# Performance work log

Hardware: AMD Instinct MI355X
Metric: run time of the kernel (lower is better)

The kernel has to match this reference:

```python
import jax, jax.numpy as jnp
import numpy as np

B, S, H, L, NH, DH, FF = 64, 256, 768, 12, 12, 64, 3072
V, MAXP, NTYPE, NI, NS = 30522, 512, 2, 10, 64


def setup_inputs() -> dict:
    key = jax.random.key(0)
    ks = iter(jax.random.split(key, 40))
    n = lambda shp, s=0.02: jax.random.normal(next(ks), shp, jnp.float32) * s
    inp = {
        'input_ids': jax.random.randint(next(ks), (B, S), 0, V),
        'attention_mask': jnp.ones((B, S), jnp.int32),
        'token_type_ids': jnp.zeros((B, S), jnp.int32),
        'intent_labels': jax.random.randint(next(ks), (B,), 0, NI),
        'slot_labels': jax.random.randint(next(ks), (B, S), 0, NS),
        'word_emb': n((V, H)), 'pos_emb': n((MAXP, H)), 'type_emb': n((NTYPE, H)),
        'emb_ln_g': jnp.ones((H,)), 'emb_ln_b': jnp.zeros((H,)),
        'Wq': n((L, H, H)), 'bq': jnp.zeros((L, H)),
        'Wk': n((L, H, H)), 'bk': jnp.zeros((L, H)),
        'Wv': n((L, H, H)), 'bv': jnp.zeros((L, H)),
        'Wo': n((L, H, H)), 'bo': jnp.zeros((L, H)),
        'ln1_g': jnp.ones((L, H)), 'ln1_b': jnp.zeros((L, H)),
        'W1': n((L, H, FF)), 'b1': jnp.zeros((L, FF)),
        'W2': n((L, FF, H)), 'b2': jnp.zeros((L, H)),
        'ln2_g': jnp.ones((L, H)), 'ln2_b': jnp.zeros((L, H)),
        'Wi': n((H, NI)), 'bi': jnp.zeros((NI,)),
        'Ws': n((H, NS)), 'bs': jnp.zeros((NS,)),
        'crf_start': n((NS,), 0.1), 'crf_end': n((NS,), 0.1),
        'crf_trans': n((NS, NS), 0.1),
    }
    return inp


def _ln(x, g, b):
    m = x.mean(-1, keepdims=True)
    v = jnp.square(x - m).mean(-1, keepdims=True)
    return (x - m) * jax.lax.rsqrt(v + 1e-12) * g + b


def _forward(params, input_ids, attention_mask, token_type_ids, intent_labels, slot_labels):
    (word_emb, pos_emb, type_emb, emb_ln_g, emb_ln_b,
     Wq, bq, Wk, bk, Wv, bv, Wo, bo, ln1_g, ln1_b,
     W1, b1, W2, b2, ln2_g, ln2_b,
     Wi, bi, Ws, bs, crf_start, crf_end, crf_trans) = params
    Bn, Sn = input_ids.shape
    Hn = word_emb.shape[1]
    dh = Hn // NH
    # BERT embeddings (dropout is identity in eval)
    x = word_emb[input_ids] + pos_emb[:Sn][None] + type_emb[token_type_ids]
    x = _ln(x, emb_ln_g, emb_ln_b)
    bias = (1.0 - attention_mask.astype(x.dtype))[:, None, None, :] * -1e9  # [B,1,1,S]

    def layer(h, p):
        wq, cq, wk, ck, wv, cv, wo, co, g1, d1, w1, e1, w2, e2, g2, d2 = p
        q = (h @ wq + cq).reshape(Bn, Sn, NH, dh)
        k = (h @ wk + ck).reshape(Bn, Sn, NH, dh)
        v = (h @ wv + cv).reshape(Bn, Sn, NH, dh)
        sc = jnp.einsum('bqnd,bknd->bnqk', q, k) / jnp.sqrt(jnp.float32(dh)) + bias
        a = jax.nn.softmax(sc, axis=-1)
        ctx = jnp.einsum('bnqk,bknd->bqnd', a, v).reshape(Bn, Sn, Hn)
        h2 = _ln(h + ctx @ wo + co, g1, d1)
        ff = jax.nn.gelu(h2 @ w1 + e1, approximate=False)
        return _ln(h2 + ff @ w2 + e2, g2, d2), None

    x, _ = jax.lax.scan(layer, x, (Wq, bq, Wk, bk, Wv, bv, Wo, bo,
                                   ln1_g, ln1_b, W1, b1, W2, b2, ln2_g, ln2_b))
    intent_logits = x[:, 0, :] @ Wi + bi           # [B, NI]
    slot_logits = x @ Ws + bs                      # [B, S, NS]
    # intent cross-entropy (mean over batch)
    lp = jax.nn.log_softmax(intent_logits, axis=-1)
    intent_loss = -jnp.take_along_axis(lp, intent_labels[:, None], axis=1).mean()
    # CRF log-likelihood
    mask = attention_mask.astype(slot_logits.dtype)
    em, tags = slot_logits, slot_labels
    t0 = tags[:, 0]
    score = crf_start[t0] + jnp.take_along_axis(em[:, 0, :], t0[:, None], axis=1)[:, 0]
    prev, cur = tags[:, :-1], tags[:, 1:]
    step_sc = crf_trans[prev, cur] + jnp.take_along_axis(em[:, 1:, :], cur[..., None], axis=2)[..., 0]
    score = score + (step_sc * mask[:, 1:]).sum(1)
    lengths = attention_mask.sum(1)
    last_tag = jnp.take_along_axis(tags, (lengths - 1)[:, None].astype(tags.dtype), axis=1)[:, 0]
    score = score + crf_end[last_tag]
    em_t = jnp.swapaxes(em, 0, 1)    # [S,B,C]
    mk_t = jnp.swapaxes(mask, 0, 1)  # [S,B]
    alpha0 = crf_start[None, :] + em_t[0]

    def crf_step(alpha, xs):
        e, m = xs
        nxt = jax.scipy.special.logsumexp(alpha[:, :, None] + crf_trans[None], axis=1) + e
        return jnp.where(m[:, None] > 0, nxt, alpha), None

    alpha, _ = jax.lax.scan(crf_step, alpha0, (em_t[1:], mk_t[1:]))
    logZ = jax.scipy.special.logsumexp(alpha + crf_end[None, :], axis=1)
    llh = score - logZ                # per-sequence log-likelihood
    crf_loss = -llh.mean()
    return intent_loss + 2.0 * crf_loss


def reference(input_ids, attention_mask, token_type_ids, intent_labels, slot_labels,
              word_emb, pos_emb, type_emb, emb_ln_g, emb_ln_b,
              Wq, bq, Wk, bk, Wv, bv, Wo, bo, ln1_g, ln1_b,
              W1, b1, W2, b2, ln2_g, ln2_b,
              Wi, bi, Ws, bs, crf_start, crf_end, crf_trans):
    params = (word_emb, pos_emb, type_emb, emb_ln_g, emb_ln_b,
              Wq, bq, Wk, bk, Wv, bv, Wo, bo, ln1_g, ln1_b,
              W1, b1, W2, b2, ln2_g, ln2_b,
              Wi, bi, Ws, bs, crf_start, crf_end, crf_trans)
    return _forward(params, input_ids, attention_mask, token_type_ids, intent_labels, slot_labels)
```

## Files before the change

### kernel.cpp

```cpp
#include <hip/hip_runtime.h>
#include <stdint.h>

typedef unsigned short u16;
typedef __attribute__((ext_vector_type(8))) short bh8;
typedef __attribute__((ext_vector_type(4))) float f4;

#define DEV static __device__ __forceinline__

DEV u16 f2bf(float f){ union{float f; uint32_t u;} v; v.f=f; uint32_t r=v.u + 0x7FFFu + ((v.u>>16)&1u); return (u16)(r>>16); }
DEV float bf2f(u16 u){ union{uint32_t u; float f;} v; v.u=((uint32_t)u)<<16; return v.f; }

DEV void mfma16(f4& d, bh8 a, bh8 b){
  asm("v_mfma_f32_16x16x32_bf16 %0, %1, %2, %0" : "+v"(d) : "v"(a), "v"(b));
}

#define FENCE16(A) asm volatile("s_nop 7\ns_nop 7" : \
 "+v"(A[0][0]),"+v"(A[0][1]),"+v"(A[0][2]),"+v"(A[0][3]),\
 "+v"(A[1][0]),"+v"(A[1][1]),"+v"(A[1][2]),"+v"(A[1][3]),\
 "+v"(A[2][0]),"+v"(A[2][1]),"+v"(A[2][2]),"+v"(A[2][3]),\
 "+v"(A[3][0]),"+v"(A[3][1]),"+v"(A[3][2]),"+v"(A[3][3]))

#define GLD16(g,l) __builtin_amdgcn_global_load_lds( \
    (__attribute__((address_space(1))) void*)(void*)(g), \
    (__attribute__((address_space(3))) void*)(void*)(l), 16, 0, 0)

struct GemmP { const u16* A; const u16* B; int K; void* C; int ldc;
               const float* b0; const float* b1; const float* b2; const u16* res; };

template<int EPI>
__global__ __launch_bounds__(256)
void gemm_bt(GemmP p){
  __shared__ __align__(16) u16 As[128*32];
  __shared__ __align__(16) u16 Bs[128*32];
  const int t=threadIdx.x, l=t&63, w=t>>6, wr=w>>1, wc=w&1;
  const int m0=blockIdx.x*128, n0=blockIdx.y*128;
  const u16* Ab = p.A + (size_t)m0*p.K;
  const u16* Bb = p.B + (size_t)n0*p.K;
  const int srow=l>>2, scol=(l&3)*8;
  f4 acc[4][4] = {};
  for(int k0=0;k0<p.K;k0+=32){
#pragma unroll
    for(int i=0;i<2;i++){
      const int c=w*2+i;
      GLD16(Ab + (size_t)(c*16+srow)*p.K + k0 + scol, &As[c*512]);
      GLD16(Bb + (size_t)(c*16+srow)*p.K + k0 + scol, &Bs[c*512]);
    }
    __syncthreads();
    bh8 af[4], bfr[4];
#pragma unroll
    for(int m=0;m<4;m++) af[m] = *(const bh8*)&As[(wr*64+m*16+(l&15))*32 + (l>>4)*8];
#pragma unroll
    for(int n=0;n<4;n++) bfr[n] = *(const bh8*)&Bs[(wc*64+n*16+(l&15))*32 + (l>>4)*8];
#pragma unroll
    for(int m=0;m<4;m++)
#pragma unroll
      for(int n=0;n<4;n++) mfma16(acc[m][n], af[m], bfr[n]);
    __syncthreads();
  }
  FENCE16(acc);
  const int lc=l&15, lr=(l>>4)*4;
#pragma unroll
  for(int m=0;m<4;m++)
#pragma unroll
  for(int n=0;n<4;n++)
#pragma unroll
  for(int r=0;r<4;r++){
    const int gr = m0 + wr*64 + m*16 + lr + r;
    const int gc = n0 + wc*64 + n*16 + lc;
    float v = acc[m][n][r];
    if(EPI==0){
      const float* bp = (gc<768)? p.b0 : (gc<1536? p.b1 : p.b2);
      const int bc = (gc<768)? gc : (gc<1536? gc-768 : gc-1536);
      ((u16*)p.C)[(size_t)gr*p.ldc + gc] = f2bf(v + bp[bc]);
    } else if(EPI==1){
      v += p.b0[gc] + bf2f(p.res[(size_t)gr*p.ldc + gc]);
      ((u16*)p.C)[(size_t)gr*p.ldc + gc] = f2bf(v);
    } else if(EPI==2){
      v += p.b0[gc];
      v = 0.5f*v*(1.f + erff(v*0.70710678118f));
      ((u16*)p.C)[(size_t)gr*p.ldc + gc] = f2bf(v);
    } else {
      v += (gc<64)? p.b0[gc] : 0.f;
      ((float*)p.C)[(size_t)gr*p.ldc + gc] = v;
    }
  }
}

__global__ __launch_bounds__(256)
void attn_kernel(const u16* __restrict__ qkv, const int* __restrict__ amask, u16* __restrict__ ctx){
  __shared__ __align__(16) u16 Ks[256*64];
  __shared__ __align__(16) u16 Vt[64*256];
  __shared__ __align__(16) u16 Ps[4*64*64];
  __shared__ float biasS[256];
  const int t=threadIdx.x, l=t&63, w=t>>6;
  const int b=blockIdx.x/12, h=blockIdx.x%12;
  biasS[t] = (1.f - (float)amask[b*256+t]) * -1e9f;
  const u16* kb = qkv + ((size_t)b*256)*2304 + 768 + h*64;
  const u16* vb = kb + 768;
#pragma unroll
  for(int i=0;i<8;i++){
    const int c = t + i*256;
    const int row = c>>3, seg = c&7;
    uint4 kv = *(const uint4*)(kb + (size_t)row*2304 + seg*8);
    const int ba = row*128 + seg*16;
    *(uint4*)((char*)Ks + (ba ^ ((row&7)<<4))) = kv;
    uint4 vv = *(const uint4*)(vb + (size_t)row*2304 + seg*8);
    const u16* pv = (const u16*)&vv;
#pragma unroll
    for(int j=0;j<8;j++){
      const int d = seg*8+j;
      const int bb = d*512 + row*2;
      *(u16*)((char*)Vt + (bb ^ ((d&7)<<4))) = pv[j];
    }
  }
  bh8 aq[4][2];
  const u16* qb = qkv + ((size_t)b*256 + w*64)*2304 + h*64;
#pragma unroll
  for(int m=0;m<4;m++)
#pragma unroll
    for(int ks=0;ks<2;ks++)
      aq[m][ks] = *(const bh8*)(qb + (size_t)(m*16+(l&15))*2304 + ks*32 + (l>>4)*8);
  __syncthreads();
  float mrun[4][4], lrun[4][4];
  f4 o[4][4] = {};
#pragma unroll
  for(int m=0;m<4;m++)
#pragma unroll
    for(int r=0;r<4;r++){ mrun[m][r] = -3e38f; lrun[m][r]=0.f; }
  u16* Pw = Ps + w*4096;
  for(int kt=0;kt<4;kt++){
    f4 sacc[4][4] = {};
#pragma unroll
    for(int ks=0;ks<2;ks++)
#pragma unroll
      for(int n=0;n<4;n++){
        const int row = kt*64 + n*16 + (l&15);
        const int by = row*128 + ks*64 + (l>>4)*16;
        bh8 bk = *(const bh8*)((const char*)Ks + (by ^ ((row&7)<<4)));
#pragma unroll
        for(int m=0;m<4;m++) mfma16(sacc[m][n], aq[m][ks], bk);
      }
    FENCE16(sacc);
#pragma unroll
    for(int m=0;m<4;m++){
      float rmax[4] = {-3e38f,-3e38f,-3e38f,-3e38f};
#pragma unroll
      for(int n=0;n<4;n++){
        const float bi = biasS[kt*64 + n*16 + (l&15)];
#pragma unroll
        for(int r=0;r<4;r++){
          float sv = sacc[m][n][r]*0.125f + bi;
          sacc[m][n][r] = sv;
          rmax[r] = fmaxf(rmax[r], sv);
        }
      }
#pragma unroll
      for(int dd=1; dd<16; dd<<=1)
#pragma unroll
        for(int r=0;r<4;r++) rmax[r] = fmaxf(rmax[r], __shfl_xor(rmax[r], dd));
      float psum[4];
#pragma unroll
      for(int r=0;r<4;r++){
        const float mn = fmaxf(mrun[m][r], rmax[r]);
        const float corr = __expf(mrun[m][r] - mn);
        mrun[m][r] = mn;
        lrun[m][r] *= corr;
#pragma unroll
        for(int nd=0; nd<4; nd++) o[m][nd][r] *= corr;
        psum[r] = 0.f;
      }
#pragma unroll
      for(int n=0;n<4;n++)
#pragma unroll
        for(int r=0;r<4;r++){
          const float pvv = __expf(sacc[m][n][r] - mrun[m][r]);
          sacc[m][n][r] = pvv;
          psum[r] += pvv;
        }
#pragma unroll
      for(int dd=1; dd<16; dd<<=1)
#pragma unroll
        for(int r=0;r<4;r++) psum[r] += __shfl_xor(psum[r], dd);
#pragma unroll
      for(int r=0;r<4;r++) lrun[m][r] += psum[r];
#pragma unroll
      for(int n=0;n<4;n++)
#pragma unroll
        for(int r=0;r<4;r++){
          const int prow = m*16 + (l>>4)*4 + r;
          const int pcol = n*16 + (l&15);
          const int by = prow*128 + pcol*2;
          *(u16*)((char*)Pw + (by ^ ((prow&7)<<4))) = f2bf(sacc[m][n][r]);
        }
    }
#pragma unroll
    for(int ks=0;ks<2;ks++){
      bh8 ap[4];
#pragma unroll
      for(int m=0;m<4;m++){
        const int prow = m*16 + (l&15);
        const int by = prow*128 + (ks*32 + (l>>4)*8)*2;
        ap[m] = *(const bh8*)((const char*)Pw + (by ^ ((prow&7)<<4)));
      }
#pragma unroll
      for(int nd=0; nd<4; nd++){
        const int dR = nd*16 + (l&15);
        const int by = dR*512 + (kt*64 + ks*32 + (l>>4)*8)*2;
        bh8 bv = *(const bh8*)((const char*)Vt + (by ^ ((dR&7)<<4)));
#pragma unroll
        for(int m=0;m<4;m++) mfma16(o[m][nd], ap[m], bv);
      }
    }
  }
  FENCE16(o);
#pragma unroll
  for(int m=0;m<4;m++)
#pragma unroll
  for(int nd=0; nd<4; nd++)
#pragma unroll
  for(int r=0;r<4;r++){
    const int row = w*64 + m*16 + (l>>4)*4 + r;
    const float vv = o[m][nd][r] / lrun[m][r];
    ctx[((size_t)b*256 + row)*768 + h*64 + nd*16 + (l&15)] = f2bf(vv);
  }
}

__global__ void ln_kernel(const u16* __restrict__ in, const float* __restrict__ g,
                          const float* __restrict__ b, u16* __restrict__ out){
  const int row = blockIdx.x, t = threadIdx.x;
  __shared__ float red[8];
  const u16* rp = in + (size_t)row*768;
  float v[3]; float s=0.f, q=0.f;
#pragma unroll
  for(int i=0;i<3;i++){ float x = bf2f(rp[t + i*256]); v[i]=x; s+=x; q+=x*x; }
#pragma unroll
  for(int dd=1; dd<64; dd<<=1){ s += __shfl_xor(s,dd); q += __shfl_xor(q,dd); }
  if((t&63)==0){ red[t>>6]=s; red[4+(t>>6)]=q; }
  __syncthreads();
  s = red[0]+red[1]+red[2]+red[3];
  q = red[4]+red[5]+red[6]+red[7];
  const float mean = s*(1.f/768.f);
  float var = q*(1.f/768.f) - mean*mean; var = fmaxf(var, 0.f);
  const float rs = rsqrtf(var + 1e-12f);
  u16* op = out + (size_t)row*768;
#pragma unroll
  for(int i=0;i<3;i++){ const int hh=t+i*256; op[hh] = f2bf((v[i]-mean)*rs*g[hh] + b[hh]); }
}

__global__ void embed_ln(const int* __restrict__ ids, const int* __restrict__ tti,
    const float* __restrict__ we, const float* __restrict__ pe, const float* __restrict__ te,
    const float* __restrict__ g, const float* __restrict__ bb, u16* __restrict__ x){
  const int tok = blockIdx.x, t = threadIdx.x;
  __shared__ float red[8];
  const int id = ids[tok], tyid = tti[tok], s0 = tok & 255;
  float v[3]; float s=0.f,q=0.f;
#pragma unroll
  for(int i=0;i<3;i++){
    const int hh = t+i*256;
    float x0 = we[(size_t)id*768+hh] + pe[(size_t)s0*768+hh] + te[(size_t)tyid*768+hh];
    v[i]=x0; s+=x0; q+=x0*x0;
  }
#pragma unroll
  for(int dd=1; dd<64; dd<<=1){ s += __shfl_xor(s,dd); q += __shfl_xor(q,dd); }
  if((t&63)==0){ red[t>>6]=s; red[4+(t>>6)]=q; }
  __syncthreads();
  s = red[0]+red[1]+red[2]+red[3];
  q = red[4]+red[5]+red[6]+red[7];
  const float mean = s*(1.f/768.f);
  float var = q*(1.f/768.f) - mean*mean; var = fmaxf(var, 0.f);
  const float rs = rsqrtf(var + 1e-12f);
#pragma unroll
  for(int i=0;i<3;i++){ const int hh=t+i*256; x[(size_t)tok*768+hh] = f2bf((v[i]-mean)*rs*g[hh] + bb[hh]); }
}

__global__ void transpose_cvt(const float* __restrict__ src, u16* __restrict__ dst, int R, int C){
  __shared__ float sm[32][33];
  const int ntc = C>>5;
  const int tr = blockIdx.x/ntc, tc = blockIdx.x - tr*ntc;
  const int r0 = tr<<5, c0 = tc<<5;
  const int tx = threadIdx.x, ty2 = threadIdx.y;
#pragma unroll
  for(int i=0;i<4;i++) sm[ty2+i*8][tx] = src[(size_t)(r0+ty2+i*8)*C + c0+tx];
  __syncthreads();
#pragma unroll
  for(int i=0;i<4;i++) dst[(size_t)(c0+ty2+i*8)*R + r0+tx] = f2bf(sm[tx][ty2+i*8]);
}

__global__ void conv_layer(const float* __restrict__ Wq, const float* __restrict__ Wk,
    const float* __restrict__ Wv, const float* __restrict__ Wo,
    const float* __restrict__ W1, const float* __restrict__ W2, u16* __restrict__ Wt){
  __shared__ float sm[32][33];
  const int bid = blockIdx.x;
  const float* src; u16* dst; int R, C, tt;
  if(bid<2304){
    R=768; C=768; const int mi = bid/576; tt = bid - mi*576;
    src = (mi==0?Wq: mi==1?Wk: mi==2?Wv: Wo);
    dst = Wt + (size_t)mi*589824;
  } else if(bid<4608){ R=768; C=3072; tt=bid-2304; src=W1; dst=Wt+2359296; }
  else { R=3072; C=768; tt=bid-4608; src=W2; dst=Wt+4718592; }
  const int ntc=C>>5; const int tr=tt/ntc, tc=tt-tr*ntc;
  const int r0=tr<<5, c0=tc<<5, tx=threadIdx.x, ty2=threadIdx.y;
#pragma unroll
  for(int i=0;i<4;i++) sm[ty2+i*8][tx] = src[(size_t)(r0+ty2+i*8)*C + c0+tx];
  __syncthreads();
#pragma unroll
  for(int i=0;i<4;i++) dst[(size_t)(c0+ty2+i*8)*R + r0+tx] = f2bf(sm[tx][ty2+i*8]);
}

__global__ void intent_kernel(const u16* __restrict__ x, const float* __restrict__ Wi,
    const float* __restrict__ bi, const int* __restrict__ lab, float* __restrict__ parts){
  const int b = blockIdx.x, t = threadIdx.x;
  __shared__ float xs[768];
  __shared__ float lg[10];
  const u16* rp = x + ((size_t)b*256)*768;
#pragma unroll
  for(int i=0;i<3;i++) xs[t+i*256] = bf2f(rp[t+i*256]);
  __syncthreads();
  if(t<10){
    float s = bi[t];
    for(int k=0;k<768;k++) s += xs[k]*Wi[(size_t)k*10 + t];
    lg[t] = s;
  }
  __syncthreads();
  if(t==0){
    float m = lg[0];
    for(int j=1;j<10;j++) m = fmaxf(m, lg[j]);
    float se = 0.f;
    for(int j=0;j<10;j++) se += expf(lg[j]-m);
    parts[b] = (logf(se) + m) - lg[lab[b]];
  }
}

__global__ __launch_bounds__(64)
void crf_kernel(const float* __restrict__ em, const int* __restrict__ tags,
    const int* __restrict__ amask, const float* __restrict__ cs, const float* __restrict__ ce,
    const float* __restrict__ tr, float* __restrict__ parts){
  const int b = blockIdx.x, j = threadIdx.x;
  const float* eb = em + (size_t)b*256*128;
  const int* tg = tags + b*256;
  const int* mk = amask + b*256;
  __shared__ __align__(16) float aS[64];
  float Etr[64];
#pragma unroll
  for(int i=0;i<64;i++) Etr[i] = __expf(tr[i*64 + j]);
  float sc = 0.f; int len = 0;
  for(int s=j+1; s<256; s+=64){
    const int pv = tg[s-1], cu = tg[s];
    sc += (tr[pv*64+cu] + eb[(size_t)s*128+cu]) * (float)mk[s];
  }
  for(int s=j; s<256; s+=64) len += mk[s];
#pragma unroll
  for(int dd=1; dd<64; dd<<=1){ sc += __shfl_xor(sc,dd); len += __shfl_xor(len,dd); }
  const int t0 = tg[0];
  float score = sc + cs[t0] + eb[t0] + ce[tg[len-1]];
  float a = __expf(cs[j] + eb[j]);
  float logc = 0.f;
  float em_s = eb[128 + j];
  int   mk_s = mk[1];
  for(int s=1; s<256; s++){
    const int sn = (s<255)? s+1 : s;
    const float em_n = eb[(size_t)sn*128 + j];
    const int   mk_n = mk[sn];
    aS[j] = a;
    __syncthreads();
    float acc0=0.f, acc1=0.f, acc2=0.f, acc3=0.f;
    const float4* ap = (const float4*)aS;
#pragma unroll
    for(int q2=0;q2<16;q2++){
      const float4 av = ap[q2];
      acc0 += av.x*Etr[4*q2+0];
      acc1 += av.y*Etr[4*q2+1];
      acc2 += av.z*Etr[4*q2+2];
      acc3 += av.w*Etr[4*q2+3];
    }
    __syncthreads();
    const float nxt = ((acc0+acc1)+(acc2+acc3)) * __expf(em_s);
    a = (mk_s > 0) ? nxt : a;
    if((s&7)==7){
      const float c = __shfl(a, 0);
      logc += __logf(c);
      a *= (1.f/c);
    }
    em_s = em_n; mk_s = mk_n;
  }
  float v2 = logf(a) + logc + ce[j];
  float am2 = v2;
#pragma unroll
  for(int dd=1; dd<64; dd<<=1) am2 = fmaxf(am2, __shfl_xor(am2,dd));
  float se = __expf(v2 - am2);
#pragma unroll
  for(int dd=1; dd<64; dd<<=1) se += __shfl_xor(se,dd);
  if(j==0) parts[64+b] = (logf(se)+am2) - score;
}

__global__ void final_reduce(const float* __restrict__ parts, float* __restrict__ out){
  const int t = threadIdx.x;
  float a = parts[t], c = parts[64+t];
#pragma unroll
  for(int dd=1; dd<64; dd<<=1){ a += __shfl_xor(a,dd); c += __shfl_xor(c,dd); }
  if(t==0) out[0] = a*(1.f/64.f) + 2.f*c*(1.f/64.f);
}

extern "C" void kernel_launch(void* const* d_in, const int* in_sizes, int n_in,
                              void* d_out, int out_size, void* d_ws, size_t ws_size,
                              hipStream_t stream){
  (void)in_sizes; (void)n_in; (void)out_size;
  const int* ids   = (const int*)d_in[0];
  const int* amask = (const int*)d_in[1];
  const int* tti   = (const int*)d_in[2];
  const int* ilab  = (const int*)d_in[3];
  const int* slab  = (const int*)d_in[4];
  const float* we  = (const float*)d_in[5];
  const float* pe  = (const float*)d_in[6];
  const float* te  = (const float*)d_in[7];
  const float* eg  = (const float*)d_in[8];
  const float* ebt = (const float*)d_in[9];
  const float* Wq  = (const float*)d_in[10];
  const float* bq  = (const float*)d_in[11];
  const float* Wk  = (const float*)d_in[12];
  const float* bkk = (const float*)d_in[13];
  const float* Wv  = (const float*)d_in[14];
  const float* bvv = (const float*)d_in[15];
  const float* Wo  = (const float*)d_in[16];
  const float* bo  = (const float*)d_in[17];
  const float* l1g = (const float*)d_in[18];
  const float* l1b = (const float*)d_in[19];
  const float* W1  = (const float*)d_in[20];
  const float* b1  = (const float*)d_in[21];
  const float* W2  = (const float*)d_in[22];
  const float* b2  = (const float*)d_in[23];
  const float* l2g = (const float*)d_in[24];
  const float* l2b = (const float*)d_in[25];
  const float* Wi  = (const float*)d_in[26];
  const float* bi  = (const float*)d_in[27];
  const float* Wsp = (const float*)d_in[28];
  const float* bs  = (const float*)d_in[29];
  const float* cs  = (const float*)d_in[30];
  const float* ce  = (const float*)d_in[31];
  const float* ctr = (const float*)d_in[32];

  char* ws = (char*)d_ws;
  size_t off = 0;
  auto alloc = [&](size_t bytes)->void*{ void* p = ws + off; off += (bytes+255)&~(size_t)255; return p; };
  u16* x     = (u16*)alloc(16384ull*768*2);
  u16* h2    = (u16*)alloc(16384ull*768*2);
  u16* y     = (u16*)alloc(16384ull*768*2);
  u16* qkv   = (u16*)alloc(16384ull*2304*2);
  u16* cf    = (u16*)alloc(16384ull*3072*2);
  u16* Wt    = (u16*)alloc(7077888ull*2);
  u16* WsT   = (u16*)alloc(128ull*768*2);
  float* slots = (float*)alloc(16384ull*128*4);
  float* parts = (float*)alloc(512);
  if(off > ws_size) return;

  dim3 T256(256), T328(32,8);
  embed_ln<<<dim3(16384), T256, 0, stream>>>(ids, tti, we, pe, te, eg, ebt, x);
  transpose_cvt<<<dim3(48), T328, 0, stream>>>(Wsp, WsT, 768, 64);
  for(int L=0; L<12; L++){
    const size_t oH = (size_t)L*768*768, oF = (size_t)L*768*3072;
    conv_layer<<<dim3(6912), T328, 0, stream>>>(Wq+oH, Wk+oH, Wv+oH, Wo+oH, W1+oF, W2+oF, Wt);
    GemmP pq{ x, Wt, 768, qkv, 2304, bq+L*768, bkk+L*768, bvv+L*768, nullptr };
    gemm_bt<0><<<dim3(128,18), T256, 0, stream>>>(pq);
    attn_kernel<<<dim3(768), T256, 0, stream>>>(qkv, amask, cf);
    GemmP po{ cf, Wt+1769472, 768, y, 768, bo+L*768, nullptr, nullptr, x };
    gemm_bt<1><<<dim3(128,6), T256, 0, stream>>>(po);
    ln_kernel<<<dim3(16384), T256, 0, stream>>>(y, l1g+L*768, l1b+L*768, h2);
    GemmP p1{ h2, Wt+2359296, 768, cf, 3072, b1+L*3072, nullptr, nullptr, nullptr };
    gemm_bt<2><<<dim3(128,24), T256, 0, stream>>>(p1);
    GemmP p2{ cf, Wt+4718592, 3072, y, 768, b2+L*768, nullptr, nullptr, h2 };
    gemm_bt<1><<<dim3(128,6), T256, 0, stream>>>(p2);
    ln_kernel<<<dim3(16384), T256, 0, stream>>>(y, l2g+L*768, l2b+L*768, x);
  }
  GemmP psl{ x, WsT, 768, slots, 128, bs, nullptr, nullptr, nullptr };
  gemm_bt<3><<<dim3(128,1), T256, 0, stream>>>(psl);
  intent_kernel<<<dim3(64), T256, 0, stream>>>(x, Wi, bi, ilab, parts);
  crf_kernel<<<dim3(64), dim3(64), 0, stream>>>(slots, slab, amask, cs, ce, ctr, parts);
  final_reduce<<<dim3(1), dim3(64), 0, stream>>>(parts, (float*)d_out);
}
```

Before: 5.481 ms.

## Replace encoder GEMMs with 256x256-tile double-buffered swizzled LDS kernel

Adds a new GEMM kernel with 256x256 output tiles, 512 threads, BK=64, double-buffered LDS staging through direct global-to-LDS loads, XOR-swizzled LDS layout, and interleaved prefetch of stage k+2 between MFMA phases with priority hints. All four per-layer GEMMs (QKV, output projection, FFN1, FFN2) switch to it, while the old kernel stays only for the slot classifier. The aim is higher arithmetic intensity per tile, fewer LDS bank conflicts and overlap of memory loads with MFMA work. In exchange it uses 128KB of dynamic shared memory per block, so occupancy drops to about one block per CU. The grids also get smaller, for example 192 blocks for the N=768 GEMMs, which can leave CUs idle.

```diff
diff --git a/kernel.cpp b/kernel.cpp
--- a/kernel.cpp
+++ b/kernel.cpp
@@ -28,44 +28,120 @@
                const float* b0; const float* b1; const float* b2; const u16* res; };
 
 template<int EPI>
-__global__ __launch_bounds__(256)
-void gemm_bt(GemmP p){
-  __shared__ __align__(16) u16 As[128*32];
-  __shared__ __align__(16) u16 Bs[128*32];
-  const int t=threadIdx.x, l=t&63, w=t>>6, wr=w>>1, wc=w&1;
-  const int m0=blockIdx.x*128, n0=blockIdx.y*128;
-  const u16* Ab = p.A + (size_t)m0*p.K;
-  const u16* Bb = p.B + (size_t)n0*p.K;
-  const int srow=l>>2, scol=(l&3)*8;
-  f4 acc[4][4] = {};
-  for(int k0=0;k0<p.K;k0+=32){
-#pragma unroll
-    for(int i=0;i<2;i++){
-      const int c=w*2+i;
-      GLD16(Ab + (size_t)(c*16+srow)*p.K + k0 + scol, &As[c*512]);
-      GLD16(Bb + (size_t)(c*16+srow)*p.K + k0 + scol, &Bs[c*512]);
-    }
-    __syncthreads();
-    bh8 af[4], bfr[4];
-#pragma unroll
-    for(int m=0;m<4;m++) af[m] = *(const bh8*)&As[(wr*64+m*16+(l&15))*32 + (l>>4)*8];
-#pragma unroll
-    for(int n=0;n<4;n++) bfr[n] = *(const bh8*)&Bs[(wc*64+n*16+(l&15))*32 + (l>>4)*8];
-#pragma unroll
-    for(int m=0;m<4;m++)
-#pragma unroll
-      for(int n=0;n<4;n++) mfma16(acc[m][n], af[m], bfr[n]);
-    __syncthreads();
-  }
-  FENCE16(acc);
-  const int lc=l&15, lr=(l>>4)*4;
-#pragma unroll
-  for(int m=0;m<4;m++)
+__global__ __launch_bounds__(512)
+void gemm256(GemmP p){
+  extern __shared__ char smem[];
+  const int t=threadIdx.x, l=t&63, w=t>>6;
+  const int wr=w>>2, wc=w&3;
+  const int m0=blockIdx.x*256, n0=blockIdx.y*256;
+  const int K=p.K, NT=K>>6;
+
+  const int off0 = w*1024 + l*16;
+  const int r0 = off0>>7;
+  const int r1 = r0 + 64;
+  const int cs = ((((off0&127)>>4) ^ (r0&7))*16);
+  const char* Ag = (const char*)p.A;
+  const char* Bg = (const char*)p.B;
+
+  #define STAGE_A(kt,h,buf) do{ \
+    char* _d = smem + (buf)*65536 + (h)*16384 + w*1024; \
+    GLD16(Ag + ((size_t)(m0 + (h)*128 + r0)*K + (kt)*64)*2 + cs, _d); \
+    GLD16(Ag + ((size_t)(m0 + (h)*128 + r1)*K + (kt)*64)*2 + cs, _d + 8192); }while(0)
+  #define STAGE_B(kt,h,buf) do{ \
+    char* _d = smem + (buf)*65536 + 32768 + (h)*16384 + w*1024; \
+    GLD16(Bg + ((size_t)(n0 + (h)*128 + r0)*K + (kt)*64)*2 + cs, _d); \
+    GLD16(Bg + ((size_t)(n0 + (h)*128 + r1)*K + (kt)*64)*2 + cs, _d + 8192); }while(0)
+
+  const int fl = l&15, fh = l>>4;
+  #define LDA(buf,mf,ks) (*(const bh8*)(smem + (buf)*65536 + (wr*128 + (mf)*16 + fl)*128 + \
+      (((ks)*64 + fh*16) ^ (((wr*128 + (mf)*16 + fl)&7)<<4))))
+  #define LDB(buf,nf,ks) (*(const bh8*)(smem + (buf)*65536 + 32768 + (wc*64 + (nf)*16 + fl)*128 + \
+      (((ks)*64 + fh*16) ^ (((wc*64 + (nf)*16 + fl)&7)<<4))))
+
+  f4 acc[8][4] = {};
+  bh8 bf_[4][2], af_[2][2];
+
+  STAGE_B(0,0,0); STAGE_B(0,1,0); STAGE_A(0,0,0); STAGE_A(0,1,0);
+  if(NT>1){ STAGE_B(1,0,1); STAGE_B(1,1,1); STAGE_A(1,0,1); STAGE_A(1,1,1);
+            asm volatile("s_waitcnt vmcnt(8)" ::: "memory"); }
+  else    { asm volatile("s_waitcnt vmcnt(0)" ::: "memory"); }
+  __builtin_amdgcn_s_barrier();
+
+  for(int h=0; h<NT; ++h){
+    const int cur = h&1;
+    const bool st = (h+2)<NT;
+#pragma unroll
+    for(int n=0;n<4;n++){ bf_[n][0]=LDB(cur,n,0); bf_[n][1]=LDB(cur,n,1); }
+    af_[0][0]=LDA(cur,0,0); af_[0][1]=LDA(cur,0,1);
+    af_[1][0]=LDA(cur,1,0); af_[1][1]=LDA(cur,1,1);
+    if(st) STAGE_B(h+2,0,cur);
+    __builtin_amdgcn_s_barrier();
+    asm volatile("s_waitcnt lgkmcnt(0)" ::: "memory");
+    __builtin_amdgcn_sched_barrier(0);
+    __builtin_amdgcn_s_setprio(1);
+#pragma unroll
+    for(int j=0;j<2;j++)
+#pragma unroll
+      for(int n=0;n<4;n++){ mfma16(acc[j][n], af_[j][0], bf_[n][0]); mfma16(acc[j][n], af_[j][1], bf_[n][1]); }
+    __builtin_amdgcn_s_setprio(0);
+    __builtin_amdgcn_s_barrier();
+    af_[0][0]=LDA(cur,2,0); af_[0][1]=LDA(cur,2,1);
+    af_[1][0]=LDA(cur,3,0); af_[1][1]=LDA(cur,3,1);
+    if(st) STAGE_B(h+2,1,cur);
+    __builtin_amdgcn_s_barrier();
+    asm volatile("s_waitcnt lgkmcnt(0)" ::: "memory");
+    __builtin_amdgcn_sched_barrier(0);
+    __builtin_amdgcn_s_setprio(1);
+#pragma unroll
+    for(int j=0;j<2;j++)
+#pragma unroll
+      for(int n=0;n<4;n++){ mfma16(acc[2+j][n], af_[j][0], bf_[n][0]); mfma16(acc[2+j][n], af_[j][1], bf_[n][1]); }
+    __builtin_amdgcn_s_setprio(0);
+    __builtin_amdgcn_s_barrier();
+    af_[0][0]=LDA(cur,4,0); af_[0][1]=LDA(cur,4,1);
+    af_[1][0]=LDA(cur,5,0); af_[1][1]=LDA(cur,5,1);
+    __builtin_amdgcn_s_barrier();
+    asm volatile("s_waitcnt lgkmcnt(0)" ::: "memory");
+    __builtin_amdgcn_sched_barrier(0);
+    __builtin_amdgcn_s_setprio(1);
+#pragma unroll
+    for(int j=0;j<2;j++)
+#pragma unroll
+      for(int n=0;n<4;n++){ mfma16(acc[4+j][n], af_[j][0], bf_[n][0]); mfma16(acc[4+j][n], af_[j][1], bf_[n][1]); }
+    __builtin_amdgcn_s_setprio(0);
+    __builtin_amdgcn_s_barrier();
+    af_[0][0]=LDA(cur,6,0); af_[0][1]=LDA(cur,6,1);
+    af_[1][0]=LDA(cur,7,0); af_[1][1]=LDA(cur,7,1);
+    if(st){ STAGE_A(h+2,0,cur); STAGE_A(h+2,1,cur);
+            asm volatile("s_waitcnt vmcnt(6)" ::: "memory"); }
+    else if(h+1<NT){ asm volatile("s_waitcnt vmcnt(0)" ::: "memory"); }
+    __builtin_amdgcn_s_barrier();
+    asm volatile("s_waitcnt lgkmcnt(0)" ::: "memory");
+    __builtin_amdgcn_sched_barrier(0);
+    __builtin_amdgcn_s_setprio(1);
+#pragma unroll
+    for(int j=0;j<2;j++)
+#pragma unroll
+      for(int n=0;n<4;n++){ mfma16(acc[6+j][n], af_[j][0], bf_[n][0]); mfma16(acc[6+j][n], af_[j][1], bf_[n][1]); }
+    __builtin_amdgcn_s_setprio(0);
+    __builtin_amdgcn_s_barrier();
+  }
+  #undef STAGE_A
+  #undef STAGE_B
+  #undef LDA
+  #undef LDB
+  asm volatile("s_nop 7\ns_nop 7" :
+    "+v"(acc[6][0]),"+v"(acc[6][1]),"+v"(acc[6][2]),"+v"(acc[6][3]),
+    "+v"(acc[7][0]),"+v"(acc[7][1]),"+v"(acc[7][2]),"+v"(acc[7][3]));
+
+  const int lc=fl, lr=fh*4;
+#pragma unroll
+  for(int m=0;m<8;m++)
 #pragma unroll
   for(int n=0;n<4;n++)
 #pragma unroll
   for(int r=0;r<4;r++){
-    const int gr = m0 + wr*64 + m*16 + lr + r;
+    const int gr = m0 + wr*128 + m*16 + lr + r;
     const int gc = n0 + wc*64 + n*16 + lc;
     float v = acc[m][n][r];
     if(EPI==0){
@@ -80,6 +156,54 @@
       v = 0.5f*v*(1.f + erff(v*0.70710678118f));
       ((u16*)p.C)[(size_t)gr*p.ldc + gc] = f2bf(v);
     } else {
+      v += (gc<64)? p.b0[gc] : 0.f;
+      ((float*)p.C)[(size_t)gr*p.ldc + gc] = v;
+    }
+  }
+}
+
+template<int EPI>
+__global__ __launch_bounds__(256)
+void gemm_bt(GemmP p){
+  __shared__ __align__(16) u16 As[128*32];
+  __shared__ __align__(16) u16 Bs[128*32];
+  const int t=threadIdx.x, l=t&63, w=t>>6, wr=w>>1, wc=w&1;
+  const int m0=blockIdx.x*128, n0=blockIdx.y*128;
+  const u16* Ab = p.A + (size_t)m0*p.K;
+  const u16* Bb = p.B + (size_t)n0*p.K;
+  const int srow=l>>2, scol=(l&3)*8;
+  f4 acc[4][4] = {};
+  for(int k0=0;k0<p.K;k0+=32){
+#pragma unroll
+    for(int i=0;i<2;i++){
+      const int c=w*2+i;
+      GLD16(Ab + (size_t)(c*16+srow)*p.K + k0 + scol, &As[c*512]);
+      GLD16(Bb + (size_t)(c*16+srow)*p.K + k0 + scol, &Bs[c*512]);
+    }
+    __syncthreads();
+    bh8 af[4], bfr[4];
+#pragma unroll
+    for(int m=0;m<4;m++) af[m] = *(const bh8*)&As[(wr*64+m*16+(l&15))*32 + (l>>4)*8];
+#pragma unroll
+    for(int n=0;n<4;n++) bfr[n] = *(const bh8*)&Bs[(wc*64+n*16+(l&15))*32 + (l>>4)*8];
+#pragma unroll
+    for(int m=0;m<4;m++)
+#pragma unroll
+      for(int n=0;n<4;n++) mfma16(acc[m][n], af[m], bfr[n]);
+    __syncthreads();
+  }
+  FENCE16(acc);
+  const int lc=l&15, lr=(l>>4)*4;
+#pragma unroll
+  for(int m=0;m<4;m++)
+#pragma unroll
+  for(int n=0;n<4;n++)
+#pragma unroll
+  for(int r=0;r<4;r++){
+    const int gr = m0 + wr*64 + m*16 + lr + r;
+    const int gc = n0 + wc*64 + n*16 + lc;
+    float v = acc[m][n][r];
+    if(EPI==3){
       v += (gc<64)? p.b0[gc] : 0.f;
       ((float*)p.C)[(size_t)gr*p.ldc + gc] = v;
     }
@@ -453,22 +577,26 @@
   float* parts = (float*)alloc(512);
   if(off > ws_size) return;
 
-  dim3 T256(256), T328(32,8);
+  (void)hipFuncSetAttribute((const void*)gemm256<0>, hipFuncAttributeMaxDynamicSharedMemorySize, 131072);
+  (void)hipFuncSetAttribute((const void*)gemm256<1>, hipFuncAttributeMaxDynamicSharedMemorySize, 131072);
+  (void)hipFuncSetAttribute((const void*)gemm256<2>, hipFuncAttributeMaxDynamicSharedMemorySize, 131072);
+
+  dim3 T256(256), T512(512), T328(32,8);
   embed_ln<<<dim3(16384), T256, 0, stream>>>(ids, tti, we, pe, te, eg, ebt, x);
   transpose_cvt<<<dim3(48), T328, 0, stream>>>(Wsp, WsT, 768, 64);
   for(int L=0; L<12; L++){
     const size_t oH = (size_t)L*768*768, oF = (size_t)L*768*3072;
     conv_layer<<<dim3(6912), T328, 0, stream>>>(Wq+oH, Wk+oH, Wv+oH, Wo+oH, W1+oF, W2+oF, Wt);
     GemmP pq{ x, Wt, 768, qkv, 2304, bq+L*768, bkk+L*768, bvv+L*768, nullptr };
-    gemm_bt<0><<<dim3(128,18), T256, 0, stream>>>(pq);
+    gemm256<0><<<dim3(64,9), T512, 131072, stream>>>(pq);
     attn_kernel<<<dim3(768), T256, 0, stream>>>(qkv, amask, cf);
     GemmP po{ cf, Wt+1769472, 768, y, 768, bo+L*768, nullptr, nullptr, x };
-    gemm_bt<1><<<dim3(128,6), T256, 0, stream>>>(po);
+    gemm256<1><<<dim3(64,3), T512, 131072, stream>>>(po);
     ln_kernel<<<dim3(16384), T256, 0, stream>>>(y, l1g+L*768, l1b+L*768, h2);
     GemmP p1{ h2, Wt+2359296, 768, cf, 3072, b1+L*3072, nullptr, nullptr, nullptr };
-    gemm_bt<2><<<dim3(128,24), T256, 0, stream>>>(p1);
+    gemm256<2><<<dim3(64,12), T512, 131072, stream>>>(p1);
     GemmP p2{ cf, Wt+4718592, 3072, y, 768, b2+L*768, nullptr, nullptr, h2 };
-    gemm_bt<1><<<dim3(128,6), T256, 0, stream>>>(p2);
+    gemm256<1><<<dim3(64,3), T512, 131072, stream>>>(p2);
     ln_kernel<<<dim3(16384), T256, 0, stream>>>(y, l2g+L*768, l2b+L*768, x);
   }
   GemmP psl{ x, WsT, 768, slots, 128, bs, nullptr, nullptr, nullptr };
```

Measured after the change: 5.775 ms. 1.05x slower.
